# Kernel optimization log

Hardware: AMD Instinct MI355X
Metric: run time of the kernel (lower is better)

## Reference

```python
import jax, jax.numpy as jnp
import numpy as np
from jax import lax

EPS = 1e-12  # torch F.normalize default eps


def _l2_normalize(x):
    # normalize over channel dim (axis=1), matching F.normalize(p=2, dim=1)
    norm = jnp.sqrt(jnp.sum(x * x, axis=1, keepdims=True))
    return x / jnp.maximum(norm, EPS)


def setup_inputs() -> dict:
    key = jax.random.key(0)
    k1, k2 = jax.random.split(key)
    B, C, H, W = 4, 256, 128, 256
    left_features = jax.random.normal(k1, (B, C, H, W), dtype=jnp.float32)
    right_features = jax.random.normal(k2, (B, C, H, W), dtype=jnp.float32)
    return {"left_features": left_features, "right_features": right_features,
            "max_displacement": 48}


def reference(left_features, right_features, max_displacement):
    L = _l2_normalize(left_features)
    R = _l2_normalize(right_features)
    D = max_displacement
    B, C, H, W = L.shape
    # pad right features with D-1 zero columns on the left so that
    # slice starting at (D-1-i) gives R shifted right by i (zeros fill-in)
    Rpad = jnp.pad(R, ((0, 0), (0, 0), (0, 0), (D - 1, 0)))
    # loop over the small fixed displacement set; each term is a fused
    # multiply + channel reduction producing [B, H, W]
    corr = [jnp.sum(L * lax.dynamic_slice_in_dim(Rpad, D - 1 - i, W, axis=3), axis=1)
            for i in range(D)]
    return jnp.stack(corr, axis=1)  # [B, D, H, W]
```

## Files before the change

### kernel.cpp

```cpp
#include <hip/hip_runtime.h>

#define NB 4
#define NC 256
#define NH 128
#define NW 256
#define ND 48
#define NHW (NH * NW)
#define CC 32
#define NCHUNK (NC / CC)
#define RW (NW + ND)

__device__ inline void async16(void* lds, const void* g) {
  __builtin_amdgcn_global_load_lds(
      (const __attribute__((address_space(1))) void*)g,
      (__attribute__((address_space(3))) void*)lds,
      16, 0, 0);
}

__global__ __launch_bounds__(256, 2)
void corr_vol_kernel(const float* __restrict__ Lf,
                     const float* __restrict__ Rf,
                     float* __restrict__ out) {
  __shared__ float Lt[CC][NW];
  __shared__ float Rt[CC][RW];
  __shared__ float nL[NW];
  __shared__ float nR[RW];

  const int tid  = threadIdx.x;
  const int lane = tid & 63;
  const int wv   = tid >> 6;
  const int b    = blockIdx.x >> 7;
  const int h    = blockIdx.x & 127;

  const float* Lb = Lf + ((size_t)b * NC) * NHW + (size_t)h * NW;
  const float* Rb = Rf + ((size_t)b * NC) * NHW + (size_t)h * NW;

  for (int idx = tid; idx < CC * ND; idx += 256) {
    Rt[idx / ND][idx % ND] = 0.0f;
  }
  if (tid < ND) nR[tid] = 0.0f;

  const int w0 = (tid & 63) << 2;
  const int i0 = (tid >> 6) * 12;
  const int rb = w0 + 36 - i0;

  float acc[4][12];
  #pragma unroll
  for (int a = 0; a < 4; ++a)
    #pragma unroll
    for (int q = 0; q < 12; ++q) acc[a][q] = 0.0f;

  float l2 = 0.0f, r2 = 0.0f;

  for (int ch = 0; ch < NCHUNK; ++ch) {
    const size_t coff = (size_t)(ch * CC) * NHW;
    #pragma unroll
    for (int k = 0; k < 8; ++k) {
      const int cl = wv * 8 + k;
      const size_t go = coff + (size_t)cl * NHW + (size_t)(lane * 4);
      async16(&Lt[cl][0],  Lb + go);
      async16(&Rt[cl][ND], Rb + go);
    }
    __syncthreads();

    #pragma unroll 8
    for (int c = 0; c < CC; ++c) {
      const float lv = Lt[c][tid];
      const float rv = Rt[c][tid + ND];
      l2 = fmaf(lv, lv, l2);
      r2 = fmaf(rv, rv, r2);
    }

    #pragma unroll 4
    for (int c = 0; c < CC; ++c) {
      const float4 lv4 = *reinterpret_cast<const float4*>(&Lt[c][w0]);
      const float4 r0v = *reinterpret_cast<const float4*>(&Rt[c][rb]);
      const float4 r1v = *reinterpret_cast<const float4*>(&Rt[c][rb + 4]);
      const float4 r2v = *reinterpret_cast<const float4*>(&Rt[c][rb + 8]);
      const float4 r3v = *reinterpret_cast<const float4*>(&Rt[c][rb + 12]);
      const float ll[4] = {lv4.x, lv4.y, lv4.z, lv4.w};
      const float rr[16] = {r0v.x, r0v.y, r0v.z, r0v.w,
                            r1v.x, r1v.y, r1v.z, r1v.w,
                            r2v.x, r2v.y, r2v.z, r2v.w,
                            r3v.x, r3v.y, r3v.z, r3v.w};
      #pragma unroll
      for (int dw = 0; dw < 4; ++dw) {
        #pragma unroll
        for (int di = 0; di < 12; ++di) {
          acc[dw][di] = fmaf(ll[dw], rr[dw - di + 12], acc[dw][di]);
        }
      }
    }
    __syncthreads();
  }

  nL[tid] = l2;
  nR[tid + ND] = r2;
  __syncthreads();

  float invL[4];
  #pragma unroll
  for (int a = 0; a < 4; ++a)
    invL[a] = 1.0f / fmaxf(sqrtf(nL[w0 + a]), 1e-12f);

  const int jb = w0 - i0 + ND;
  float invR[15];
  #pragma unroll
  for (int k = 0; k < 15; ++k)
    invR[k] = 1.0f / fmaxf(sqrtf(nR[jb - 11 + k]), 1e-12f);

  #pragma unroll
  for (int di = 0; di < 12; ++di) {
    const int i = i0 + di;
    float4 v;
    v.x = acc[0][di] * invL[0] * invR[0 - di + 11];
    v.y = acc[1][di] * invL[1] * invR[1 - di + 11];
    v.z = acc[2][di] * invL[2] * invR[2 - di + 11];
    v.w = acc[3][di] * invL[3] * invR[3 - di + 11];
    *reinterpret_cast<float4*>(out + ((size_t)(b * ND + i) * NH + h) * NW + w0) = v;
  }
}

extern "C" void kernel_launch(void* const* d_in, const int* in_sizes, int n_in,
                              void* d_out, int out_size, void* d_ws, size_t ws_size,
                              hipStream_t stream) {
  const float* Lf = (const float*)d_in[0];
  const float* Rf = (const float*)d_in[1];
  float* out = (float*)d_out;
  dim3 grid(NB * NH);
  dim3 block(256);
  corr_vol_kernel<<<grid, block, 0, stream>>>(Lf, Rf, out);
}
```

Measured before the change: 294.5 us.

## Double-buffer channel chunks with async LDS loads to overlap loads and compute

Halves the channel chunk size and allocates two LDS buffers for L and R tiles. The next chunk is prefetched with async global-to-LDS loads while the current one is computed, and manual vmcnt waits plus raw barriers replace __syncthreads. The goal is to hide global load latency behind the FMA work. In exchange it doubles the number of barrier phases, and the manual waitcnt accounting must match the number of outstanding loads.

```diff
diff --git a/kernel.cpp b/kernel.cpp
--- a/kernel.cpp
+++ b/kernel.cpp
@@ -6,7 +6,7 @@
 #define NW 256
 #define ND 48
 #define NHW (NH * NW)
-#define CC 32
+#define CC 16
 #define NCHUNK (NC / CC)
 #define RW (NW + ND)
 
@@ -21,8 +21,8 @@
 void corr_vol_kernel(const float* __restrict__ Lf,
                      const float* __restrict__ Rf,
                      float* __restrict__ out) {
-  __shared__ float Lt[CC][NW];
-  __shared__ float Rt[CC][RW];
+  __shared__ float Lt[2][CC][NW];
+  __shared__ float Rt[2][CC][RW];
   __shared__ float nL[NW];
   __shared__ float nR[RW];
 
@@ -35,10 +35,13 @@
   const float* Lb = Lf + ((size_t)b * NC) * NHW + (size_t)h * NW;
   const float* Rb = Rf + ((size_t)b * NC) * NHW + (size_t)h * NW;
 
-  for (int idx = tid; idx < CC * ND; idx += 256) {
-    Rt[idx / ND][idx % ND] = 0.0f;
+  for (int idx = tid; idx < 2 * CC * ND; idx += 256) {
+    const int bufi = idx / (CC * ND);
+    const int rem  = idx % (CC * ND);
+    Rt[bufi][rem / ND][rem % ND] = 0.0f;
   }
   if (tid < ND) nR[tid] = 0.0f;
+  __syncthreads();
 
   const int w0 = (tid & 63) << 2;
   const int i0 = (tid >> 6) * 12;
@@ -52,32 +55,47 @@
 
   float l2 = 0.0f, r2 = 0.0f;
 
-  for (int ch = 0; ch < NCHUNK; ++ch) {
-    const size_t coff = (size_t)(ch * CC) * NHW;
-    #pragma unroll
-    for (int k = 0; k < 8; ++k) {
-      const int cl = wv * 8 + k;
-      const size_t go = coff + (size_t)cl * NHW + (size_t)(lane * 4);
-      async16(&Lt[cl][0],  Lb + go);
-      async16(&Rt[cl][ND], Rb + go);
+  #pragma unroll
+  for (int j = 0; j < 4; ++j) {
+    const int cl = wv * 4 + j;
+    const size_t go = (size_t)cl * NHW + (size_t)(lane * 4);
+    async16(&Lt[0][cl][0],  Lb + go);
+    async16(&Rt[0][cl][ND], Rb + go);
+  }
+
+  for (int k = 0; k < NCHUNK; ++k) {
+    const int cur = k & 1;
+    if (k + 1 < NCHUNK) {
+      const int nxt = cur ^ 1;
+      const size_t coff = (size_t)((k + 1) * CC) * NHW;
+      #pragma unroll
+      for (int j = 0; j < 4; ++j) {
+        const int cl = wv * 4 + j;
+        const size_t go = coff + (size_t)cl * NHW + (size_t)(lane * 4);
+        async16(&Lt[nxt][cl][0],  Lb + go);
+        async16(&Rt[nxt][cl][ND], Rb + go);
+      }
+      asm volatile("s_waitcnt vmcnt(8)" ::: "memory");
+    } else {
+      asm volatile("s_waitcnt vmcnt(0)" ::: "memory");
     }
-    __syncthreads();
+    __builtin_amdgcn_s_barrier();
 
     #pragma unroll 8
     for (int c = 0; c < CC; ++c) {
-      const float lv = Lt[c][tid];
-      const float rv = Rt[c][tid + ND];
+      const float lv = Lt[cur][c][tid];
+      const float rv = Rt[cur][c][tid + ND];
       l2 = fmaf(lv, lv, l2);
       r2 = fmaf(rv, rv, r2);
     }
 
     #pragma unroll 4
     for (int c = 0; c < CC; ++c) {
-      const float4 lv4 = *reinterpret_cast<const float4*>(&Lt[c][w0]);
-      const float4 r0v = *reinterpret_cast<const float4*>(&Rt[c][rb]);
-      const float4 r1v = *reinterpret_cast<const float4*>(&Rt[c][rb + 4]);
-      const float4 r2v = *reinterpret_cast<const float4*>(&Rt[c][rb + 8]);
-      const float4 r3v = *reinterpret_cast<const float4*>(&Rt[c][rb + 12]);
+      const float4 lv4 = *reinterpret_cast<const float4*>(&Lt[cur][c][w0]);
+      const float4 r0v = *reinterpret_cast<const float4*>(&Rt[cur][c][rb]);
+      const float4 r1v = *reinterpret_cast<const float4*>(&Rt[cur][c][rb + 4]);
+      const float4 r2v = *reinterpret_cast<const float4*>(&Rt[cur][c][rb + 8]);
+      const float4 r3v = *reinterpret_cast<const float4*>(&Rt[cur][c][rb + 12]);
       const float ll[4] = {lv4.x, lv4.y, lv4.z, lv4.w};
       const float rr[16] = {r0v.x, r0v.y, r0v.z, r0v.w,
                             r1v.x, r1v.y, r1v.z, r1v.w,
@@ -91,7 +109,7 @@
         }
       }
     }
-    __syncthreads();
+    __builtin_amdgcn_s_barrier();
   }
 
   nL[tid] = l2;
```

New measurement: 342.8 us. 16.4% more time.

## Drop LDS staging and load features directly from global memory per thread

Applied to the files above, without the earlier changes.

Removes the shared-memory tiles, the async global-to-LDS copies and the block barriers. Each thread now reads its left float4 and four right float4 windows straight from global memory for every channel. Each thread also computes its own channel-norm sums in registers, instead of sharing them through LDS. Out-of-range right columns are clamped to a valid address, and the affected outputs are masked to zero. This trades barrier and LDS traffic for redundant global and L1 loads and extra per-thread norm FMAs.

```diff
diff --git a/kernel.cpp b/kernel.cpp
--- a/kernel.cpp
+++ b/kernel.cpp
@@ -6,117 +6,77 @@
 #define NW 256
 #define ND 48
 #define NHW (NH * NW)
-#define CC 32
-#define NCHUNK (NC / CC)
-#define RW (NW + ND)
-
-__device__ inline void async16(void* lds, const void* g) {
-  __builtin_amdgcn_global_load_lds(
-      (const __attribute__((address_space(1))) void*)g,
-      (__attribute__((address_space(3))) void*)lds,
-      16, 0, 0);
-}
 
 __global__ __launch_bounds__(256, 2)
 void corr_vol_kernel(const float* __restrict__ Lf,
                      const float* __restrict__ Rf,
                      float* __restrict__ out) {
-  __shared__ float Lt[CC][NW];
-  __shared__ float Rt[CC][RW];
-  __shared__ float nL[NW];
-  __shared__ float nR[RW];
+  const int tid = threadIdx.x;
+  const int b   = blockIdx.x >> 7;
+  const int h   = blockIdx.x & 127;
+  const int w0  = (tid & 63) << 2;
+  const int i0  = (tid >> 6) * 12;
 
-  const int tid  = threadIdx.x;
-  const int lane = tid & 63;
-  const int wv   = tid >> 6;
-  const int b    = blockIdx.x >> 7;
-  const int h    = blockIdx.x & 127;
-
-  const float* Lb = Lf + ((size_t)b * NC) * NHW + (size_t)h * NW;
-  const float* Rb = Rf + ((size_t)b * NC) * NHW + (size_t)h * NW;
-
-  for (int idx = tid; idx < CC * ND; idx += 256) {
-    Rt[idx / ND][idx % ND] = 0.0f;
-  }
-  if (tid < ND) nR[tid] = 0.0f;
-
-  const int w0 = (tid & 63) << 2;
-  const int i0 = (tid >> 6) * 12;
-  const int rb = w0 + 36 - i0;
+  const int rowbase = (b * NC * NH + h) * NW;
+  int lOff = rowbase + w0;
+  int rOff = rowbase + w0 - i0 - 12;
 
   float acc[4][12];
+  float l2[4] = {0.f, 0.f, 0.f, 0.f};
+  float r2[16];
+  #pragma unroll
+  for (int q = 0; q < 16; ++q) r2[q] = 0.f;
   #pragma unroll
   for (int a = 0; a < 4; ++a)
     #pragma unroll
-    for (int q = 0; q < 12; ++q) acc[a][q] = 0.0f;
+    for (int d = 0; d < 12; ++d) acc[a][d] = 0.f;
 
-  float l2 = 0.0f, r2 = 0.0f;
+  #pragma unroll 2
+  for (int c = 0; c < NC; ++c) {
+    const float4 lv  = *reinterpret_cast<const float4*>(Lf + lOff);
+    const float4 rq0 = *reinterpret_cast<const float4*>(Rf + (rOff      > 0 ? rOff      : 0));
+    const float4 rq1 = *reinterpret_cast<const float4*>(Rf + (rOff + 4  > 0 ? rOff + 4  : 0));
+    const float4 rq2 = *reinterpret_cast<const float4*>(Rf + (rOff + 8  > 0 ? rOff + 8  : 0));
+    const float4 rq3 = *reinterpret_cast<const float4*>(Rf + (rOff + 12 > 0 ? rOff + 12 : 0));
+    lOff += NHW;
+    rOff += NHW;
 
-  for (int ch = 0; ch < NCHUNK; ++ch) {
-    const size_t coff = (size_t)(ch * CC) * NHW;
+    const float ll[4]  = {lv.x, lv.y, lv.z, lv.w};
+    const float rr[16] = {rq0.x, rq0.y, rq0.z, rq0.w,
+                          rq1.x, rq1.y, rq1.z, rq1.w,
+                          rq2.x, rq2.y, rq2.z, rq2.w,
+                          rq3.x, rq3.y, rq3.z, rq3.w};
+
     #pragma unroll
-    for (int k = 0; k < 8; ++k) {
-      const int cl = wv * 8 + k;
-      const size_t go = coff + (size_t)cl * NHW + (size_t)(lane * 4);
-      async16(&Lt[cl][0],  Lb + go);
-      async16(&Rt[cl][ND], Rb + go);
-    }
-    __syncthreads();
+    for (int a = 0; a < 4; ++a) l2[a] = fmaf(ll[a], ll[a], l2[a]);
+    #pragma unroll
+    for (int q = 1; q < 16; ++q) r2[q] = fmaf(rr[q], rr[q], r2[q]);
 
-    #pragma unroll 8
-    for (int c = 0; c < CC; ++c) {
-      const float lv = Lt[c][tid];
-      const float rv = Rt[c][tid + ND];
-      l2 = fmaf(lv, lv, l2);
-      r2 = fmaf(rv, rv, r2);
-    }
-
-    #pragma unroll 4
-    for (int c = 0; c < CC; ++c) {
-      const float4 lv4 = *reinterpret_cast<const float4*>(&Lt[c][w0]);
-      const float4 r0v = *reinterpret_cast<const float4*>(&Rt[c][rb]);
-      const float4 r1v = *reinterpret_cast<const float4*>(&Rt[c][rb + 4]);
-      const float4 r2v = *reinterpret_cast<const float4*>(&Rt[c][rb + 8]);
-      const float4 r3v = *reinterpret_cast<const float4*>(&Rt[c][rb + 12]);
-      const float ll[4] = {lv4.x, lv4.y, lv4.z, lv4.w};
-      const float rr[16] = {r0v.x, r0v.y, r0v.z, r0v.w,
-                            r1v.x, r1v.y, r1v.z, r1v.w,
-                            r2v.x, r2v.y, r2v.z, r2v.w,
-                            r3v.x, r3v.y, r3v.z, r3v.w};
+    #pragma unroll
+    for (int dw = 0; dw < 4; ++dw)
       #pragma unroll
-      for (int dw = 0; dw < 4; ++dw) {
-        #pragma unroll
-        for (int di = 0; di < 12; ++di) {
-          acc[dw][di] = fmaf(ll[dw], rr[dw - di + 12], acc[dw][di]);
-        }
-      }
-    }
-    __syncthreads();
+      for (int di = 0; di < 12; ++di)
+        acc[dw][di] = fmaf(ll[dw], rr[dw - di + 12], acc[dw][di]);
   }
-
-  nL[tid] = l2;
-  nR[tid + ND] = r2;
-  __syncthreads();
 
   float invL[4];
   #pragma unroll
   for (int a = 0; a < 4; ++a)
-    invL[a] = 1.0f / fmaxf(sqrtf(nL[w0 + a]), 1e-12f);
-
-  const int jb = w0 - i0 + ND;
-  float invR[15];
+    invL[a] = 1.0f / fmaxf(sqrtf(l2[a]), 1e-12f);
+  float invR[16];
+  invR[0] = 0.0f;
   #pragma unroll
-  for (int k = 0; k < 15; ++k)
-    invR[k] = 1.0f / fmaxf(sqrtf(nR[jb - 11 + k]), 1e-12f);
+  for (int q = 1; q < 16; ++q)
+    invR[q] = 1.0f / fmaxf(sqrtf(r2[q]), 1e-12f);
 
   #pragma unroll
   for (int di = 0; di < 12; ++di) {
     const int i = i0 + di;
     float4 v;
-    v.x = acc[0][di] * invL[0] * invR[0 - di + 11];
-    v.y = acc[1][di] * invL[1] * invR[1 - di + 11];
-    v.z = acc[2][di] * invL[2] * invR[2 - di + 11];
-    v.w = acc[3][di] * invL[3] * invR[3 - di + 11];
+    v.x = (w0 + 0 >= i) ? acc[0][di] * invL[0] * invR[0 - di + 12] : 0.0f;
+    v.y = (w0 + 1 >= i) ? acc[1][di] * invL[1] * invR[1 - di + 12] : 0.0f;
+    v.z = (w0 + 2 >= i) ? acc[2][di] * invL[2] * invR[2 - di + 12] : 0.0f;
+    v.w = (w0 + 3 >= i) ? acc[3][di] * invL[3] * invR[3 - di + 12] : 0.0f;
     *reinterpret_cast<float4*>(out + ((size_t)(b * ND + i) * NH + h) * NW + w0) = v;
   }
 }
```

Result: slower. 317.8 us (+7.9%).
